# Optimization experiments

Measured on AMD Instinct MI355X. Metric: run time of the kernel, lower is better.

Reference implementation:

```python
import jax, jax.numpy as jnp
import numpy as np

B, CIN, COUT, H, W = 8, 128, 128, 64, 64

# kernel-grid base offsets (dy, dx), row-major k = kh*3 + kw, matching torch base_offset-1
BASE = jnp.array([[-1, -1], [-1, 0], [-1, 1],
                  [0, -1], [0, 0], [0, 1],
                  [1, -1], [1, 0], [1, 1]], dtype=jnp.float32)  # [9,2]
CORNER = jnp.array([1, 0, 1, 0, 0, 0, 1, 0, 1], dtype=jnp.float32)  # mask1 per kernel tap
EDGE = jnp.array([0, 1, 0, 1, 0, 1, 0, 1, 0], dtype=jnp.float32)    # mask2 per kernel tap


def conv3x3(x, w, b=None):
    out = jax.lax.conv_general_dilated(
        x, w, window_strides=(1, 1), padding=((1, 1), (1, 1)),
        dimension_numbers=('NCHW', 'OIHW', 'NCHW'))
    if b is not None:
        out = out + b[None, :, None, None]
    return out


def bilinear_sample(x, py, px):
    Bv, C, Hin, Win = x.shape
    y0 = jnp.floor(py)
    x0 = jnp.floor(px)
    wy = py - y0
    wx = px - x0
    y0i = y0.astype(jnp.int32)
    x0i = x0.astype(jnp.int32)
    xf = x.reshape(Bv, C, Hin * Win)

    def corner(yi, xi):
        valid = ((yi >= 0) & (yi < Hin) & (xi >= 0) & (xi < Win)).astype(x.dtype)
        idx = jnp.clip(yi, 0, Hin - 1) * Win + jnp.clip(xi, 0, Win - 1)  # [B,K,Ho,Wo]
        g = jax.vmap(lambda xb, ib: xb[:, ib])(xf, idx)  # [B,C,K,Ho,Wo]
        return g * valid[:, None]

    v00 = corner(y0i, x0i)
    v01 = corner(y0i, x0i + 1)
    v10 = corner(y0i + 1, x0i)
    v11 = corner(y0i + 1, x0i + 1)
    wy = wy[:, None]
    wx = wx[:, None]
    return (v00 * (1 - wy) * (1 - wx) + v01 * (1 - wy) * wx
            + v10 * wy * (1 - wx) + v11 * wy * wx)


def setup_inputs() -> dict:
    key = jax.random.key(0)
    k1, k2, k3 = jax.random.split(key, 3)
    x = jax.random.normal(k1, (B, CIN, H, W), dtype=jnp.float32)
    # small offset-conv weights keep predicted offsets in a realistic sub-pixel range
    w_off = jax.random.normal(k2, (5, CIN, 3, 3), dtype=jnp.float32) * 0.02
    b_off = jnp.zeros((5,), dtype=jnp.float32)
    w = jax.random.normal(k3, (COUT, CIN, 3, 3), dtype=jnp.float32) * (1.0 / np.sqrt(CIN * 9))
    b = jnp.zeros((COUT,), dtype=jnp.float32)
    return {"x": x, "w_off": w_off, "b_off": b_off, "w": w, "b": b}


def reference(x, w_off, b_off, w, b):
    off = conv3x3(x, w_off, b_off)          # [B,5,H,W]
    scale1 = jax.nn.relu(off[:, 2:3]) + 1.0  # corner scale [B,1,H,W]
    scale2 = jax.nn.relu(off[:, 3:4]) + 1.0  # edge scale   [B,1,H,W]
    shift = off[:, :2]                       # equivariant shift vector [B,2,H,W]

    # per-tap scale; center tap gets 0 but its base offset is (0,0) anyway
    scale_k = CORNER[None, :, None, None] * scale1 + EDGE[None, :, None, None] * scale2  # [B,9,H,W]
    # deform offset = scaled_base - base + shift = base*(scale-1) + shift
    delta = BASE[None, :, :, None, None] * (scale_k - 1.0)[:, :, None] + shift[:, None]  # [B,9,2,H,W]

    hs = jnp.arange(H, dtype=x.dtype)
    ws = jnp.arange(W, dtype=x.dtype)
    # sampling positions: p0 + base_k + offset_k (stride=1, pad=1)
    py = hs[None, None, :, None] + BASE[None, :, 0, None, None] + delta[:, :, 0]  # [B,9,H,W]
    px = ws[None, None, None, :] + BASE[None, :, 1, None, None] + delta[:, :, 1]

    sampled = bilinear_sample(x, py, px)  # [B,CIN,9,H,W]
    out = jnp.einsum('bckhw,ock->bohw', sampled, w.reshape(COUT, CIN, 9))
    return out + b[None, :, None, None]
```

## Files before the change

### kernel.cpp

```cpp
#include <hip/hip_runtime.h>

#define Wd 64
#define Hd 64
#define HWp 4096
#define CIN_ 128
#define COUT_ 128

typedef _Float16 f16;
typedef _Float16 h2    __attribute__((ext_vector_type(2)));
typedef _Float16 f16x8 __attribute__((ext_vector_type(8)));
typedef float f32x4    __attribute__((ext_vector_type(4)));

__device__ inline ushort f2h(float f) {
    f16 h = (f16)f;
    return __builtin_bit_cast(ushort, h);
}
__device__ inline h2 gb(const int4& g, int d) {
    return __builtin_bit_cast(h2, (&g.x)[d]);
}
__device__ inline h2 dup(float f) {
    f16 h = (f16)f;
    h2 r; r[0] = h; r[1] = h;
    return r;
}
struct H8 { h2 r[4]; };

__global__ __launch_bounds__(256) void prep_offsets_kernel(
    const float* __restrict__ x, const float* __restrict__ w,
    const float* __restrict__ w_off, const float* __restrict__ b_off,
    ushort* __restrict__ xt, ushort* __restrict__ w_t2,
    int4* __restrict__ midx, float4* __restrict__ mw)
{
    __shared__ char smem[34816];
    int blk = blockIdx.x;
    int t = threadIdx.x;

    if (blk < 256) {
        ushort* tile = (ushort*)smem;
        int b = blk >> 5, yx0 = (blk & 31) << 7;
        const float* xb = x + (size_t)b * CIN_ * HWp + yx0;
        int lanelo = t & 31, grp = t >> 5;
        #pragma unroll
        for (int i = 0; i < 4; i++) {
            int cbase = i * 32 + grp * 4;
            float4 v0 = *(const float4*)(xb + (size_t)(cbase + 0) * HWp + lanelo * 4);
            float4 v1 = *(const float4*)(xb + (size_t)(cbase + 1) * HWp + lanelo * 4);
            float4 v2 = *(const float4*)(xb + (size_t)(cbase + 2) * HWp + lanelo * 4);
            float4 v3 = *(const float4*)(xb + (size_t)(cbase + 3) * HWp + lanelo * 4);
            ushort4 u;
            u.x = f2h(v0.x); u.y = f2h(v1.x); u.z = f2h(v2.x); u.w = f2h(v3.x);
            *(ushort4*)&tile[(lanelo * 4 + 0) * 136 + cbase] = u;
            u.x = f2h(v0.y); u.y = f2h(v1.y); u.z = f2h(v2.y); u.w = f2h(v3.y);
            *(ushort4*)&tile[(lanelo * 4 + 1) * 136 + cbase] = u;
            u.x = f2h(v0.z); u.y = f2h(v1.z); u.z = f2h(v2.z); u.w = f2h(v3.z);
            *(ushort4*)&tile[(lanelo * 4 + 2) * 136 + cbase] = u;
            u.x = f2h(v0.w); u.y = f2h(v1.w); u.z = f2h(v2.w); u.w = f2h(v3.w);
            *(ushort4*)&tile[(lanelo * 4 + 3) * 136 + cbase] = u;
        }
        __syncthreads();
        ushort* dst = xt + ((size_t)b * HWp + yx0) * CIN_;
        int c8 = (t & 15) * 8, yxg = t >> 4;
        #pragma unroll
        for (int i = 0; i < 8; i++) {
            int yxl = i * 16 + yxg;
            int4 v = *(int4*)&tile[yxl * 136 + c8];
            *(int4*)(dst + (size_t)yxl * CIN_ + c8) = v;
        }
    } else if (blk < 832) {
        int i = (blk - 256) * 256 + t;
        int j    = i & 7;
        int lane = (i >> 3) & 63;
        int ii   = (i >> 9) & 3;
        int wm   = (i >> 11) & 1;
        int s    = i >> 12;
        int o = wm * 64 + ii * 16 + (lane & 15);
        int c = (s & 3) * 32 + (lane >> 4) * 8 + j;
        int k = s >> 2;
        w_t2[i] = f2h(w[o * 1152 + c * 9 + k]);
    } else {
        float* wl   = (float*)smem;
        float* part = (float*)(smem + 18432);
        float* der  = (float*)(smem + 22528);
        int blk2 = blk - 832;
        int b = blk2 >> 6;
        int h = blk2 & 63;

        for (int i = t; i < 4608; i += 256) {
            int j = i / 1152;
            int r = i - j * 1152;
            wl[r * 4 + j] = w_off[i];
        }
        __syncthreads();

        int pi = t & 63, cc = t >> 6;
        const float* xb = x + (size_t)(b * CIN_ + cc * 32) * HWp;

        int idx9[9];
        float msk9[9];
        #pragma unroll
        for (int dy = 0; dy < 3; dy++) {
            int hy = h + dy - 1;
            int hyc = min(max(hy, 0), Hd - 1);
            bool vr = (hy >= 0) && (hy < Hd);
            #pragma unroll
            for (int dx = 0; dx < 3; dx++) {
                int wx = pi + dx - 1;
                int wxc = min(max(wx, 0), Wd - 1);
                bool v = vr && (wx >= 0) && (wx < Wd);
                idx9[dy * 3 + dx] = hyc * Wd + wxc;
                msk9[dy * 3 + dx] = v ? 1.0f : 0.0f;
            }
        }

        float o0 = 0.f, o1 = 0.f, o2 = 0.f, o3 = 0.f;
        #pragma unroll 2
        for (int c = 0; c < 32; c++) {
            const float* xp = xb + c * HWp;
            const float* wc = &wl[(cc * 32 + c) * 36];
            float xv[9];
            #pragma unroll
            for (int tp = 0; tp < 9; tp++) xv[tp] = xp[idx9[tp]] * msk9[tp];
            #pragma unroll
            for (int tp = 0; tp < 9; tp++) {
                float4 wj = *(const float4*)&wc[tp * 4];
                o0 += xv[tp] * wj.x; o1 += xv[tp] * wj.y;
                o2 += xv[tp] * wj.z; o3 += xv[tp] * wj.w;
            }
        }
        part[t * 4 + 0] = o0;
        part[t * 4 + 1] = o1;
        part[t * 4 + 2] = o2;
        part[t * 4 + 3] = o3;
        __syncthreads();

        if (t < 64) {
            float s0 = b_off[0], s1 = b_off[1], s2 = b_off[2], s3 = b_off[3];
            #pragma unroll
            for (int q = 0; q < 4; q++) {
                s0 += part[(q * 64 + t) * 4 + 0];
                s1 += part[(q * 64 + t) * 4 + 1];
                s2 += part[(q * 64 + t) * 4 + 2];
                s3 += part[(q * 64 + t) * 4 + 3];
            }
            der[t * 4 + 0] = s0;
            der[t * 4 + 1] = s1;
            der[t * 4 + 2] = fmaxf(s2, 0.f) + 1.f;
            der[t * 4 + 3] = fmaxf(s3, 0.f) + 1.f;
        }
        __syncthreads();

        #pragma unroll
        for (int s = 0; s < 3; s++) {
            int q = t + s * 256;
            if (q < 576) {
                int k = q >> 6;
                int pp = q & 63;
                float sy = der[pp * 4 + 0], sx = der[pp * 4 + 1];
                float sc1 = der[pp * 4 + 2], sc2 = der[pp * 4 + 3];
                int ky = k / 3, kx = k - ky * 3;
                float by = (float)(ky - 1), bx = (float)(kx - 1);
                bool corner = (ky != 1) && (kx != 1);
                bool edge = (ky != 1) ^ (kx != 1);
                float sk = corner ? sc1 : (edge ? sc2 : 0.0f);
                float py = (float)h + by * sk + sy;
                float px = (float)pp + bx * sk + sx;
                float y0f = floorf(py), x0f = floorf(px);
                float wy = py - y0f, wx = px - x0f;
                int y0 = (int)y0f, x0 = (int)x0f;
                int y1 = y0 + 1, x1 = x0 + 1;
                float vy0 = (y0 >= 0 && y0 < Hd) ? 1.f : 0.f;
                float vy1 = (y1 >= 0 && y1 < Hd) ? 1.f : 0.f;
                float vx0 = (x0 >= 0 && x0 < Wd) ? 1.f : 0.f;
                float vx1 = (x1 >= 0 && x1 < Wd) ? 1.f : 0.f;
                int cy0 = min(max(y0, 0), Hd - 1), cy1 = min(max(y1, 0), Hd - 1);
                int cx0 = min(max(x0, 0), Wd - 1), cx1 = min(max(x1, 0), Wd - 1);
                int4 ii;
                ii.x = cy0 * Wd + cx0;
                ii.y = cy0 * Wd + cx1;
                ii.z = cy1 * Wd + cx0;
                ii.w = cy1 * Wd + cx1;
                float4 ww;
                ww.x = (1.f - wy) * (1.f - wx) * vy0 * vx0;
                ww.y = (1.f - wy) * wx * vy0 * vx1;
                ww.z = wy * (1.f - wx) * vy1 * vx0;
                ww.w = wy * wx * vy1 * vx1;
                int addr = (b * 9 + k) * HWp + h * Wd + pp;
                midx[addr] = ii;
                mw[addr] = ww;
            }
        }
    }
}

__global__ __launch_bounds__(512, 1) void deform_gemm_mfma(
    const ushort* __restrict__ xt, const ushort* __restrict__ w_t2,
    const float* __restrict__ bias, const int4* __restrict__ midx,
    const float4* __restrict__ mw, float* __restrict__ out)
{
    __shared__ ushort A_lds[2][2][4096];
    __shared__ ushort S_lds[2][2][128 * 40];

    int t = threadIdx.x;
    int b = blockIdx.x >> 5;
    int rp = blockIdx.x & 31;
    int p0 = rp << 7;
    const ushort* xtb = xt + (size_t)b * HWp * CIN_;

    int p  = t >> 2;
    int c8 = (t & 3) << 3;

    int wv = t >> 6, lane = t & 63;
    int wm = wv & 1, ns = wv >> 1;
    int lm = lane & 15, lq = lane >> 4;

    f32x4 acc[4][2] = {};

    const ushort* cbp[4];
    h2 cwp[4];
    auto loadmeta = [&](int k) {
        int addr = (b * 9 + k) * HWp + p0 + p;
        int4 mi = midx[addr];
        float4 v = mw[addr];
        cbp[0] = xtb + mi.x * CIN_ + c8;
        cbp[1] = xtb + mi.y * CIN_ + c8;
        cbp[2] = xtb + mi.z * CIN_ + c8;
        cbp[3] = xtb + mi.w * CIN_ + c8;
        cwp[0] = dup(v.x); cwp[1] = dup(v.y);
        cwp[2] = dup(v.z); cwp[3] = dup(v.w);
    };

    auto stageA = [&](int buf, int st) {
        const ushort* src = w_t2 + (size_t)st * 8192;
        #pragma unroll
        for (int cc = 0; cc < 2; cc++) {
            const ushort* g = src + cc * 4096 + wv * 512 + lane * 8;
            ushort* l = &A_lds[buf][cc][wv * 512];
            __builtin_amdgcn_global_load_lds(
                (const __attribute__((address_space(1))) unsigned int*)g,
                (__attribute__((address_space(3))) unsigned int*)l, 16, 0, 0);
        }
    };

    int4 Gc[2][4], Gn[2][4];
    auto issue = [&](int st, int4 G[2][4]) {
        #pragma unroll
        for (int cc = 0; cc < 2; cc++) {
            int q = (2 * st + cc) & 3;
            #pragma unroll
            for (int r = 0; r < 4; r++)
                G[cc][r] = *(const int4*)(cbp[r] + q * 32);
        }
    };
    auto commitS = [&](int buf, const int4 G[2][4]) {
        #pragma unroll
        for (int cc = 0; cc < 2; cc++) {
            H8 tmp;
            #pragma unroll
            for (int d = 0; d < 4; d++) {
                h2 r = gb(G[cc][0], d) * cwp[0];
                r = gb(G[cc][1], d) * cwp[1] + r;
                r = gb(G[cc][2], d) * cwp[2] + r;
                r = gb(G[cc][3], d) * cwp[3] + r;
                tmp.r[d] = r;
            }
            *(int4*)&S_lds[buf][cc][p * 40 + c8] = __builtin_bit_cast(int4, tmp);
        }
    };

    loadmeta(0);
    issue(0, Gc);
    stageA(0, 0);
    commitS(0, Gc);
    __syncthreads();

    for (int st = 0; st < 18; st++) {
        int cur = st & 1, nb = cur ^ 1;
        bool prod = (st + 1 < 18);
        if (prod) {
            if (((st + 1) & 1) == 0) loadmeta((st + 1) >> 1);
            issue(st + 1, Gn);
            stageA(nb, st + 1);
        }

        #pragma unroll
        for (int cc = 0; cc < 2; cc++) {
            f16x8 af[4], bfr[2];
            #pragma unroll
            for (int i = 0; i < 4; i++)
                af[i] = *(const f16x8*)&A_lds[cur][cc][(wm * 4 + i) * 512 + lane * 8];
            #pragma unroll
            for (int f = 0; f < 2; f++)
                bfr[f] = *(const f16x8*)&S_lds[cur][cc][(ns * 32 + f * 16 + lm) * 40 + lq * 8];
            #pragma unroll
            for (int i = 0; i < 4; i++)
                #pragma unroll
                for (int f = 0; f < 2; f++)
                    acc[i][f] = __builtin_amdgcn_mfma_f32_16x16x32_f16(
                        af[i], bfr[f], acc[i][f], 0, 0, 0);
        }

        if (prod) {
            commitS(nb, Gn);
            #pragma unroll
            for (int cc = 0; cc < 2; cc++)
                #pragma unroll
                for (int r = 0; r < 4; r++) Gc[cc][r] = Gn[cc][r];
        }
        __syncthreads();
    }

    #pragma unroll
    for (int i = 0; i < 4; i++) {
        #pragma unroll
        for (int r = 0; r < 4; r++) {
            int o = wm * 64 + i * 16 + lq * 4 + r;
            float bv = bias[o];
            float* orow = out + (size_t)(b * COUT_ + o) * HWp + p0 + ns * 32 + lm;
            #pragma unroll
            for (int f = 0; f < 2; f++)
                orow[f * 16] = acc[i][f][r] + bv;
        }
    }
}

extern "C" void kernel_launch(void* const* d_in, const int* in_sizes, int n_in,
                              void* d_out, int out_size, void* d_ws, size_t ws_size,
                              hipStream_t stream) {
    const float* x     = (const float*)d_in[0];
    const float* w_off = (const float*)d_in[1];
    const float* b_off = (const float*)d_in[2];
    const float* w     = (const float*)d_in[3];
    const float* bias  = (const float*)d_in[4];
    float* out = (float*)d_out;

    char* ws = (char*)d_ws;
    ushort* xt   = (ushort*)ws;
    ushort* w_t2 = (ushort*)(ws + 8388608);
    int4*   midx = (int4*)(ws + 8683520);
    float4* mwp  = (float4*)(ws + 13402112);

    prep_offsets_kernel<<<1344, 256, 0, stream>>>(x, w, w_off, b_off,
                                                  xt, w_t2, midx, mwp);
    deform_gemm_mfma<<<256, 512, 0, stream>>>(xt, w_t2, bias, midx, mwp, out);
}
```

Before: 123.2 us.

## Pack sampling metadata into one int4 and halve GEMM block tile size

```diff
diff --git a/kernel.cpp b/kernel.cpp
--- a/kernel.cpp
+++ b/kernel.cpp
@@ -18,18 +18,13 @@
 __device__ inline h2 gb(const int4& g, int d) {
     return __builtin_bit_cast(h2, (&g.x)[d]);
 }
-__device__ inline h2 dup(float f) {
-    f16 h = (f16)f;
-    h2 r; r[0] = h; r[1] = h;
-    return r;
-}
 struct H8 { h2 r[4]; };
 
 __global__ __launch_bounds__(256) void prep_offsets_kernel(
     const float* __restrict__ x, const float* __restrict__ w,
     const float* __restrict__ w_off, const float* __restrict__ b_off,
     ushort* __restrict__ xt, ushort* __restrict__ w_t2,
-    int4* __restrict__ midx, float4* __restrict__ mw)
+    int4* __restrict__ meta)
 {
     __shared__ char smem[34816];
     int blk = blockIdx.x;
@@ -174,36 +169,33 @@
                 float vx1 = (x1 >= 0 && x1 < Wd) ? 1.f : 0.f;
                 int cy0 = min(max(y0, 0), Hd - 1), cy1 = min(max(y1, 0), Hd - 1);
                 int cx0 = min(max(x0, 0), Wd - 1), cx1 = min(max(x1, 0), Wd - 1);
-                int4 ii;
-                ii.x = cy0 * Wd + cx0;
-                ii.y = cy0 * Wd + cx1;
-                ii.z = cy1 * Wd + cx0;
-                ii.w = cy1 * Wd + cx1;
-                float4 ww;
-                ww.x = (1.f - wy) * (1.f - wx) * vy0 * vx0;
-                ww.y = (1.f - wy) * wx * vy0 * vx1;
-                ww.z = wy * (1.f - wx) * vy1 * vx0;
-                ww.w = wy * wx * vy1 * vx1;
-                int addr = (b * 9 + k) * HWp + h * Wd + pp;
-                midx[addr] = ii;
-                mw[addr] = ww;
+                float w0 = (1.f - wy) * (1.f - wx) * vy0 * vx0;
+                float w1 = (1.f - wy) * wx * vy0 * vx1;
+                float w2 = wy * (1.f - wx) * vy1 * vx0;
+                float w3 = wy * wx * vy1 * vx1;
+                int4 m;
+                m.x = cy0 | (cx0 << 8) | (cy1 << 16) | (cx1 << 24);
+                m.y = (int)((unsigned)f2h(w0) | ((unsigned)f2h(w1) << 16));
+                m.z = (int)((unsigned)f2h(w2) | ((unsigned)f2h(w3) << 16));
+                m.w = 0;
+                meta[(b * 9 + k) * HWp + h * Wd + pp] = m;
             }
         }
     }
 }
 
-__global__ __launch_bounds__(512, 1) void deform_gemm_mfma(
+__global__ __launch_bounds__(256, 2) void deform_gemm_mfma(
     const ushort* __restrict__ xt, const ushort* __restrict__ w_t2,
-    const float* __restrict__ bias, const int4* __restrict__ midx,
-    const float4* __restrict__ mw, float* __restrict__ out)
+    const float* __restrict__ bias, const int4* __restrict__ meta,
+    float* __restrict__ out)
 {
     __shared__ ushort A_lds[2][2][4096];
-    __shared__ ushort S_lds[2][2][128 * 40];
+    __shared__ ushort S_lds[2][2][64 * 40];
 
     int t = threadIdx.x;
-    int b = blockIdx.x >> 5;
-    int rp = blockIdx.x & 31;
-    int p0 = rp << 7;
+    int b = blockIdx.x >> 6;
+    int h = blockIdx.x & 63;
+    int p0 = h << 6;
     const ushort* xtb = xt + (size_t)b * HWp * CIN_;
 
     int p  = t >> 2;
@@ -218,27 +210,36 @@
     const ushort* cbp[4];
     h2 cwp[4];
     auto loadmeta = [&](int k) {
-        int addr = (b * 9 + k) * HWp + p0 + p;
-        int4 mi = midx[addr];
-        float4 v = mw[addr];
-        cbp[0] = xtb + mi.x * CIN_ + c8;
-        cbp[1] = xtb + mi.y * CIN_ + c8;
-        cbp[2] = xtb + mi.z * CIN_ + c8;
-        cbp[3] = xtb + mi.w * CIN_ + c8;
-        cwp[0] = dup(v.x); cwp[1] = dup(v.y);
-        cwp[2] = dup(v.z); cwp[3] = dup(v.w);
+        int4 m = meta[(b * 9 + k) * HWp + p0 + p];
+        int cy0 = m.x & 0xff, cx0 = (m.x >> 8) & 0xff;
+        int cy1 = (m.x >> 16) & 0xff, cx1 = (m.x >> 24) & 0xff;
+        int ry0 = cy0 << 13, ry1 = cy1 << 13;
+        int rx0 = cx0 << 7,  rx1 = cx1 << 7;
+        const ushort* base = xtb + c8;
+        cbp[0] = base + ry0 + rx0;
+        cbp[1] = base + ry0 + rx1;
+        cbp[2] = base + ry1 + rx0;
+        cbp[3] = base + ry1 + rx1;
+        h2 p01 = __builtin_bit_cast(h2, m.y);
+        h2 p23 = __builtin_bit_cast(h2, m.z);
+        cwp[0] = __builtin_shufflevector(p01, p01, 0, 0);
+        cwp[1] = __builtin_shufflevector(p01, p01, 1, 1);
+        cwp[2] = __builtin_shufflevector(p23, p23, 0, 0);
+        cwp[3] = __builtin_shufflevector(p23, p23, 1, 1);
     };
 
     auto stageA = [&](int buf, int st) {
         const ushort* src = w_t2 + (size_t)st * 8192;
         #pragma unroll
-        for (int cc = 0; cc < 2; cc++) {
-            const ushort* g = src + cc * 4096 + wv * 512 + lane * 8;
-            ushort* l = &A_lds[buf][cc][wv * 512];
-            __builtin_amdgcn_global_load_lds(
-                (const __attribute__((address_space(1))) unsigned int*)g,
-                (__attribute__((address_space(3))) unsigned int*)l, 16, 0, 0);
-        }
+        for (int cc = 0; cc < 2; cc++)
+            #pragma unroll
+            for (int r = 0; r < 2; r++) {
+                const ushort* g = src + cc * 4096 + (wv * 2 + r) * 512 + lane * 8;
+                ushort* l = &A_lds[buf][cc][(wv * 2 + r) * 512];
+                __builtin_amdgcn_global_load_lds(
+                    (const __attribute__((address_space(1))) unsigned int*)g,
+                    (__attribute__((address_space(3))) unsigned int*)l, 16, 0, 0);
+            }
     };
 
     int4 Gc[2][4], Gn[2][4];
@@ -336,10 +337,9 @@
     char* ws = (char*)d_ws;
     ushort* xt   = (ushort*)ws;
     ushort* w_t2 = (ushort*)(ws + 8388608);
-    int4*   midx = (int4*)(ws + 8683520);
-    float4* mwp  = (float4*)(ws + 13402112);
+    int4*   meta = (int4*)(ws + 8683520);
 
     prep_offsets_kernel<<<1344, 256, 0, stream>>>(x, w, w_off, b_off,
-                                                  xt, w_t2, midx, mwp);
-    deform_gemm_mfma<<<256, 512, 0, stream>>>(xt, w_t2, bias, midx, mwp, out);
-}
+                                                  xt, w_t2, meta);
+    deform_gemm_mfma<<<512, 256, 0, stream>>>(xt, w_t2, bias, meta, out);
+}
```

Result: slower. 125.9 us (+2.2%).
